# Optimization experiments

Hardware: AMD Instinct MI355X
Metric: run time of the kernel (lower is better)

The kernel has to match this reference:

```python
import jax, jax.numpy as jnp
import numpy as np

B, C, IMG, P = 64, 3, 224, 16
HP = IMG // P                 # 14 patches per side
N = HP * HP                   # 196 patches
R = 196                       # num_superpixels
D, HEADS, DEPTH = 384, 6, 12
HD = D // HEADS
MLP = 4 * D
CLS = 1000
WIN = 4                       # local attention window radius
SEQ = R + 1


def setup_inputs() -> dict:
    key = jax.random.key(0)
    ks = jax.random.split(key, 16)
    nrm = lambda k, s: jax.random.normal(k, s, jnp.float32) * 0.02
    return dict(
        x=jax.random.normal(ks[0], (B, C, IMG, IMG), jnp.float32),
        seg=jax.random.randint(ks[1], (B, IMG, IMG), 0, R, jnp.int32),
        patch_W=nrm(ks[2], (C * P * P, D)), patch_b=jnp.zeros((D,), jnp.float32),
        cls_token=nrm(ks[3], (1, 1, D)),
        pos_W=nrm(ks[4], (2, D)), pos_b=jnp.zeros((D,), jnp.float32),
        cls_pos=nrm(ks[5], (D,)),
        ln1_w=jnp.ones((DEPTH, D), jnp.float32), ln1_b=jnp.zeros((DEPTH, D), jnp.float32),
        qkv_W=nrm(ks[6], (DEPTH, D, 3 * D)), qkv_b=jnp.zeros((DEPTH, 3 * D), jnp.float32),
        proj_W=nrm(ks[7], (DEPTH, D, D)), proj_b=jnp.zeros((DEPTH, D), jnp.float32),
        ln2_w=jnp.ones((DEPTH, D), jnp.float32), ln2_b=jnp.zeros((DEPTH, D), jnp.float32),
        mlp_W1=nrm(ks[8], (DEPTH, D, MLP)), mlp_b1=jnp.zeros((DEPTH, MLP), jnp.float32),
        mlp_W2=nrm(ks[9], (DEPTH, MLP, D)), mlp_b2=jnp.zeros((DEPTH, D), jnp.float32),
        norm_w=jnp.ones((D,), jnp.float32), norm_b=jnp.zeros((D,), jnp.float32),
        head_W=nrm(ks[10], (D, CLS)), head_b=jnp.zeros((CLS,), jnp.float32),
    )


def _ln(x, w, b):
    m = x.mean(-1, keepdims=True)
    v = ((x - m) ** 2).mean(-1, keepdims=True)
    return (x - m) * jax.lax.rsqrt(v + 1e-5) * w + b


def _forward(x, seg, patch_W, patch_b, cls_token, pos_W, pos_b, cls_pos,
             ln1_w, ln1_b, qkv_W, qkv_b, proj_W, proj_b, ln2_w, ln2_b,
             mlp_W1, mlp_b1, mlp_W2, mlp_b2, norm_w, norm_b, head_W, head_b):
    # --- patch embedding (conv stride==kernel == patchify + matmul) -> [B,N,D]
    xp = x.reshape(B, C, HP, P, HP, P).transpose(0, 2, 4, 1, 3, 5).reshape(B, N, C * P * P)
    emb = xp @ patch_W + patch_b
    # --- patch -> superpixel id: segmentation label at patch center pixel
    centers = jnp.arange(HP) * P + P // 2
    patch_seg = seg[:, centers[:, None], centers[None, :]].reshape(B, N)
    # --- mean pooling per superpixel (fused segment reduce over all batches)
    pids = (jnp.arange(B, dtype=patch_seg.dtype)[:, None] * R + patch_seg).reshape(-1)
    sums = jax.ops.segment_sum(emb.reshape(-1, D), pids, num_segments=B * R)
    cnts = jax.ops.segment_sum(jnp.ones((B * N,), emb.dtype), pids, num_segments=B * R)
    pooled = (sums / jnp.maximum(cnts, 1.0)[:, None]).reshape(B, R, D)
    # --- superpixel centroids via pixel-level segment reduce -> [B,R,2] (x,y)
    coords = jnp.arange(IMG, dtype=jnp.float32) / IMG
    yg, xg = jnp.meshgrid(coords, coords, indexing='ij')
    gid = (jnp.arange(B, dtype=seg.dtype)[:, None] * R + seg.reshape(B, -1)).reshape(-1)
    pix = IMG * IMG
    pcnt = jax.ops.segment_sum(jnp.ones((B * pix,), jnp.float32), gid, num_segments=B * R)
    ysum = jax.ops.segment_sum(jnp.broadcast_to(yg.reshape(-1), (B, pix)).reshape(-1), gid, num_segments=B * R)
    xsum = jax.ops.segment_sum(jnp.broadcast_to(xg.reshape(-1), (B, pix)).reshape(-1), gid, num_segments=B * R)
    safe = jnp.maximum(pcnt, 1.0)
    cx = jnp.where(pcnt > 0, xsum / safe, 0.5)
    cy = jnp.where(pcnt > 0, ysum / safe, 0.5)
    centroids = jnp.stack([cx, cy], axis=-1).reshape(B, R, 2)
    # --- prepend cls token, add dynamic (centroid-based) positional encoding
    tok = jnp.concatenate([jnp.broadcast_to(cls_token, (B, 1, D)), pooled], axis=1)
    pos = jnp.concatenate([jnp.broadcast_to(cls_pos[None, None, :], (B, 1, D)),
                           centroids @ pos_W + pos_b], axis=1)
    h = tok + pos
    # --- local (banded) attention mask; cls token attends globally
    idx = jnp.arange(SEQ)
    band = jnp.abs(idx[:, None] - idx[None, :]) <= WIN
    band = band | (idx[:, None] == 0) | (idx[None, :] == 0)
    neg = jnp.float32(-1e9)
    scale = 1.0 / np.sqrt(HD)
    for l in range(DEPTH):
        z = _ln(h, ln1_w[l], ln1_b[l])
        qkv = (z @ qkv_W[l] + qkv_b[l]).reshape(B, SEQ, 3, HEADS, HD)
        q, k, v = qkv[:, :, 0], qkv[:, :, 1], qkv[:, :, 2]
        s = jnp.einsum('bqhd,bkhd->bhqk', q, k) * scale
        s = jnp.where(band[None, None], s, neg)
        a = jax.nn.softmax(s, axis=-1)
        o = jnp.einsum('bhqk,bkhd->bqhd', a, v).reshape(B, SEQ, D)
        h = h + o @ proj_W[l] + proj_b[l]
        z = _ln(h, ln2_w[l], ln2_b[l])
        h = h + jax.nn.gelu(z @ mlp_W1[l] + mlp_b1[l]) @ mlp_W2[l] + mlp_b2[l]
    h = _ln(h, norm_w, norm_b)
    return h[:, 0] @ head_W + head_b


def reference(x, seg, patch_W, patch_b, cls_token, pos_W, pos_b, cls_pos,
              ln1_w, ln1_b, qkv_W, qkv_b, proj_W, proj_b, ln2_w, ln2_b,
              mlp_W1, mlp_b1, mlp_W2, mlp_b2, norm_w, norm_b, head_W, head_b):
    return _forward(x, seg, patch_W, patch_b, cls_token, pos_W, pos_b, cls_pos,
                    ln1_w, ln1_b, qkv_W, qkv_b, proj_W, proj_b, ln2_w, ln2_b,
                    mlp_W1, mlp_b1, mlp_W2, mlp_b2, norm_w, norm_b, head_W, head_b)
```

## Files before the change

kernel.cpp:

```cpp
#include <hip/hip_runtime.h>
#include <hip/hip_bf16.h>
#include <math.h>

typedef unsigned short ushort_t;
typedef unsigned int uint_t;
typedef __attribute__((ext_vector_type(8))) short short8;
typedef __attribute__((ext_vector_type(4))) float f32x4;

#define BATCH 64
#define CHN 3
#define IMG 224
#define PATCH 16
#define HP 14
#define NPATCH 196
#define RSEG 196
#define DMODEL 384
#define HEADS 6
#define HD 64
#define DEPTH 12
#define MLPD 1536
#define CLS 1000
#define WIN 4
#define SEQ 197
#define PIX (IMG*IMG)
#define PATCHK (CHN*PATCH*PATCH)
#define CPARTS 16
#define PPP (PIX / CPARTS)

__device__ __forceinline__ ushort_t f2bf(float f) {
  uint_t u = __float_as_uint(f);
  u += 0x7FFFu + ((u >> 16) & 1u);
  return (ushort_t)(u >> 16);
}
__device__ __forceinline__ float bf2f(ushort_t u) {
  return __uint_as_float((uint_t)u << 16);
}
__device__ __forceinline__ float gelu_tanh(float x) {
  float z = 0.7978845608028654f * (x + 0.044715f * x * x * x);
  z = fminf(fmaxf(z, -15.f), 15.f);
  float t = exp2f(2.8853900817779268f * z);
  return x * t / (t + 1.f);
}
__device__ __forceinline__ int xcd_swizzle(int bid, int nwg) {
  int q = nwg >> 3, r = nwg & 7;
  int xcd = bid & 7, idx = bid >> 3;
  int start = (xcd < r) ? xcd * (q + 1) : r * (q + 1) + (xcd - r) * q;
  return start + idx;
}
__device__ __forceinline__ float dot16bf(const ushort_t* a, const ushort_t* b) {
  const uint_t* a32 = (const uint_t*)a;
  const uint_t* b32 = (const uint_t*)b;
  float acc = 0.f;
#pragma unroll
  for (int w = 0; w < 8; w++) {
    uint_t ka = a32[w], kb = b32[w];
    acc += bf2f((ushort_t)(ka & 0xffff)) * bf2f((ushort_t)(kb & 0xffff));
    acc += bf2f((ushort_t)(ka >> 16)) * bf2f((ushort_t)(kb >> 16));
  }
  return acc;
}

__global__ __launch_bounds__(256) void convtrans_kernel(
    const float* __restrict__ W, ushort_t* __restrict__ Wt, int K, int N) {
  __shared__ float t[32][33];
  int k0 = blockIdx.y * 32, n0 = blockIdx.x * 32;
  const float* Wl = W + (size_t)blockIdx.z * K * N;
  ushort_t* Wtl = Wt + (size_t)blockIdx.z * K * N;
  int tx = threadIdx.x & 31, ty = threadIdx.x >> 5;
#pragma unroll
  for (int i = 0; i < 32; i += 8)
    t[ty + i][tx] = Wl[(size_t)(k0 + ty + i) * N + n0 + tx];
  __syncthreads();
#pragma unroll
  for (int i = 0; i < 32; i += 8)
    Wtl[(size_t)(n0 + ty + i) * K + k0 + tx] = f2bf(t[tx][ty + i]);
}

__global__ __launch_bounds__(256) void patchify_kernel(
    const float* __restrict__ x, ushort_t* __restrict__ xp, int total4) {
  int idx = blockIdx.x * 256 + threadIdx.x;
  if (idx >= total4) return;
  int kq = idx % (PATCHK / 4);
  int m = idx / (PATCHK / 4);
  int n = m % NPATCH;
  int b = m / NPATCH;
  int hi = n / HP, wi = n % HP;
  int k = kq * 4;
  int c = k >> 8;
  int rem = k & 255;
  int pi = rem >> 4, pj = rem & 15;
  int row = hi * PATCH + pi, col = wi * PATCH + pj;
  f32x4 v = *(const f32x4*)&x[(((size_t)b * CHN + c) * IMG + row) * IMG + col];
  uint_t p0 = (uint_t)f2bf(v[0]) | ((uint_t)f2bf(v[1]) << 16);
  uint_t p1 = (uint_t)f2bf(v[2]) | ((uint_t)f2bf(v[3]) << 16);
  uint_t* dst = (uint_t*)(xp + (size_t)idx * 4);
  dst[0] = p0;
  dst[1] = p1;
}

template <int BMT, bool GELU, bool RESID, int OUTMODE>
__global__ __launch_bounds__(256) void gemm_gl(
    const ushort_t* __restrict__ A, const ushort_t* __restrict__ Bt,
    const float* __restrict__ bias, const float* __restrict__ resid,
    void* __restrict__ Cout, int M, int N, int K, int gx) {
  constexpr int AWS = BMT * 2;
  constexpr int AI = AWS / 64;
  constexpr int MF = 4;
  constexpr int NF = (BMT == 128) ? 4 : 2;
  constexpr int BUF_U = (BMT + 128) * 64;
  constexpr int CS_U = BMT * 136;
  constexpr int SMEM_U = (2 * BUF_U > CS_U) ? 2 * BUF_U : CS_U;
  __shared__ __align__(16) ushort_t smem[SMEM_U];
  int tid = threadIdx.x;
  int wave = tid >> 6, lane = tid & 63;
  int flat = xcd_swizzle(blockIdx.x, gridDim.x);
  int bx = flat % gx, by = flat / gx;
  int bm = by * BMT, bn = bx * 128;
  int wr = (BMT == 128) ? (wave >> 1) * 64 : 0;
  int wc = (BMT == 128) ? (wave & 1) * 64 : wave * 32;
  f32x4 acc[MF][NF];
#pragma unroll
  for (int m = 0; m < MF; m++)
#pragma unroll
    for (int n = 0; n < NF; n++)
#pragma unroll
      for (int e = 0; e < 4; e++) acc[m][n][e] = 0.f;

  int r = lane & 15;
  int cfrag = lane >> 4;

  auto STAGE = [&](int buf, int k0) {
    ushort_t* As = smem + buf * BUF_U;
    ushort_t* Bs = As + BMT * 64;
#pragma unroll
    for (int j = 0; j < AI; j++) {
      int s = wave * AWS + j * 64 + lane;
      int row = s >> 3;
      int cp = s & 7;
      int c = cp ^ ((row >> 1) & 7);
      const ushort_t* src = A + (size_t)(bm + row) * K + k0 + c * 8;
      ushort_t* dst = As + (size_t)(wave * AWS + j * 64) * 8;
      __builtin_amdgcn_global_load_lds(
          (const __attribute__((address_space(1))) void*)src,
          (__attribute__((address_space(3))) void*)dst, 16, 0, 0);
    }
#pragma unroll
    for (int j = 0; j < 4; j++) {
      int s = wave * 256 + j * 64 + lane;
      int row = s >> 3;
      int cp = s & 7;
      int c = cp ^ ((row >> 1) & 7);
      const ushort_t* src = Bt + (size_t)(bn + row) * K + k0 + c * 8;
      ushort_t* dst = Bs + (size_t)(wave * 256 + j * 64) * 8;
      __builtin_amdgcn_global_load_lds(
          (const __attribute__((address_space(1))) void*)src,
          (__attribute__((address_space(3))) void*)dst, 16, 0, 0);
    }
  };

  STAGE(0, 0);
  __syncthreads();
  int cur = 0;
  for (int k0 = 0; k0 < K; k0 += 64) {
    if (k0 + 64 < K) STAGE(cur ^ 1, k0 + 64);
    ushort_t* As = smem + cur * BUF_U;
    ushort_t* Bs = As + BMT * 64;
#pragma unroll
    for (int kk = 0; kk < 2; kk++) {
      short8 af[MF], bfr[NF];
#pragma unroll
      for (int m = 0; m < MF; m++) {
        int row = wr + m * 16 + r;
        int sl = (kk * 4 + cfrag) ^ ((row >> 1) & 7);
        af[m] = *(const short8*)(As + row * 64 + sl * 8);
      }
#pragma unroll
      for (int n = 0; n < NF; n++) {
        int row = wc + n * 16 + r;
        int sl = (kk * 4 + cfrag) ^ ((row >> 1) & 7);
        bfr[n] = *(const short8*)(Bs + row * 64 + sl * 8);
      }
      __builtin_amdgcn_s_setprio(1);
#pragma unroll
      for (int m = 0; m < MF; m++)
#pragma unroll
        for (int n = 0; n < NF; n++)
          acc[m][n] = __builtin_amdgcn_mfma_f32_16x16x32_bf16(
              af[m], bfr[n], acc[m][n], 0, 0, 0);
      __builtin_amdgcn_s_setprio(0);
    }
    __syncthreads();
    cur ^= 1;
  }
  int q4 = (lane >> 4) * 4;
  if (OUTMODE == 0) {
#pragma unroll
    for (int n = 0; n < NF; n++) {
      int col = bn + wc + n * 16 + r;
      float bi = bias[col];
#pragma unroll
      for (int m = 0; m < MF; m++) {
#pragma unroll
        for (int e = 0; e < 4; e++) {
          int row = bm + wr + m * 16 + q4 + e;
          if (row < M) {
            float v = acc[m][n][e] + bi;
            if (GELU) v = gelu_tanh(v);
            if (RESID) v += resid[(size_t)row * N + col];
            ((float*)Cout)[(size_t)row * N + col] = v;
          }
        }
      }
    }
  } else {
    ushort_t* Cs = smem;
#pragma unroll
    for (int n = 0; n < NF; n++) {
      int lc = wc + n * 16 + r;
      float bi = bias[bn + lc];
#pragma unroll
      for (int m = 0; m < MF; m++) {
#pragma unroll
        for (int e = 0; e < 4; e++) {
          int lr = wr + m * 16 + q4 + e;
          float v = acc[m][n][e] + bi;
          if (GELU) v = gelu_tanh(v);
          if (RESID) v += resid[(size_t)(bm + lr) * N + bn + lc];
          Cs[lr * 136 + lc] = f2bf(v);
        }
      }
    }
    __syncthreads();
    constexpr int CHUNKS = BMT * 16;
#pragma unroll
    for (int c = 0; c < CHUNKS / 256; c++) {
      int id = c * 256 + tid;
      int row = id >> 4, ch = id & 15;
      int grow = bm + row;
      if (grow < M) {
        short8 val = *(const short8*)(Cs + row * 136 + ch * 8);
        int gcol = bn + ch * 8;
        if (OUTMODE == 1) {
          *(short8*)((ushort_t*)Cout + (size_t)grow * N + gcol) = val;
        } else {
          int b_ = grow / SEQ, t_ = grow - b_ * SEQ;
          int which = gcol / DMODEL;
          int hcol = gcol - which * DMODEL;
          int hh = hcol >> 6, d0 = hcol & 63;
          *(short8*)((ushort_t*)Cout +
                     ((((size_t)b_ * 3 + which) * HEADS + hh) * SEQ + t_) * 64 +
                     d0) = val;
        }
      }
    }
  }
}

__global__ __launch_bounds__(256) void zeroacc_kernel(int* __restrict__ g,
                                                      int n) {
  int i = blockIdx.x * 256 + threadIdx.x;
  if (i < n) g[i] = 0;
}

__global__ __launch_bounds__(256) void centroid_part_kernel(
    const int* __restrict__ seg, int* __restrict__ gacc) {
  __shared__ int cnt[RSEG], si[RSEG], sj[RSEG];
  int b = blockIdx.x, part = blockIdx.y, tid = threadIdx.x;
  for (int r = tid; r < RSEG; r += 256) { cnt[r] = 0; si[r] = 0; sj[r] = 0; }
  __syncthreads();
  const int* s = seg + (size_t)b * PIX;
  int p0 = part * PPP;
  for (int p = p0 + tid; p < p0 + PPP; p += 256) {
    int r = s[p];
    int i = p / IMG, j = p % IMG;
    atomicAdd(&cnt[r], 1);
    atomicAdd(&si[r], i);
    atomicAdd(&sj[r], j);
  }
  __syncthreads();
  for (int r = tid; r < RSEG; r += 256) {
    int c = cnt[r];
    if (c | si[r] | sj[r]) {
      int* g = gacc + ((size_t)b * RSEG + r) * 3;
      atomicAdd(&g[0], c);
      atomicAdd(&g[1], si[r]);
      atomicAdd(&g[2], sj[r]);
    }
  }
}
__global__ __launch_bounds__(256) void centroid_fin_kernel(
    const int* __restrict__ gacc, float* __restrict__ cent) {
  int b = blockIdx.x, tid = threadIdx.x;
  for (int r = tid; r < RSEG; r += 256) {
    const int* g = gacc + ((size_t)b * RSEG + r) * 3;
    int c = g[0];
    float cx = 0.5f, cy = 0.5f;
    if (c > 0) {
      cx = ((float)g[2] / (float)IMG) / (float)c;
      cy = ((float)g[1] / (float)IMG) / (float)c;
    }
    cent[((size_t)b * RSEG + r) * 2 + 0] = cx;
    cent[((size_t)b * RSEG + r) * 2 + 1] = cy;
  }
}

__global__ __launch_bounds__(256) void patchseg_kernel(
    const int* __restrict__ seg, int* __restrict__ pseg) {
  int idx = blockIdx.x * 256 + threadIdx.x;
  if (idx >= BATCH * NPATCH) return;
  int n = idx % NPATCH, b = idx / NPATCH;
  int hi = n / HP, wi = n % HP;
  pseg[idx] = seg[(size_t)b * PIX + (8 + hi * PATCH) * IMG + (8 + wi * PATCH)];
}

__global__ __launch_bounds__(64) void buildlists_kernel(
    const int* __restrict__ pseg, int* __restrict__ starts,
    int* __restrict__ lists) {
  __shared__ int cnt[RSEG];
  int b = blockIdx.x;
  if (threadIdx.x != 0) return;
  const int* ps = pseg + b * NPATCH;
  for (int r = 0; r < RSEG; r++) cnt[r] = 0;
  for (int n = 0; n < NPATCH; n++) cnt[ps[n]]++;
  int run = 0;
  int* st = starts + b * (RSEG + 1);
  for (int r = 0; r < RSEG; r++) {
    st[r] = run;
    int c = cnt[r];
    cnt[r] = run;
    run += c;
  }
  st[RSEG] = run;
  int* li = lists + b * NPATCH;
  for (int n = 0; n < NPATCH; n++) {
    int r = ps[n];
    li[cnt[r]++] = n;
  }
}

__global__ __launch_bounds__(384) void pool_assemble_kernel(
    const float* __restrict__ emb, const float* __restrict__ cent,
    const int* __restrict__ starts, const int* __restrict__ lists,
    const float* __restrict__ cls_token, const float* __restrict__ cls_pos,
    const float* __restrict__ pos_W, const float* __restrict__ pos_b,
    float* __restrict__ h) {
  int t = blockIdx.x;
  int b = t / SEQ, s = t % SEQ;
  int d = threadIdx.x;
  float out;
  if (s == 0) {
    out = cls_token[d] + cls_pos[d];
  } else {
    int r = s - 1;
    int st = starts[b * (RSEG + 1) + r];
    int en = starts[b * (RSEG + 1) + r + 1];
    float acc = 0.f;
    for (int i = st; i < en; i++) {
      int n = lists[b * NPATCH + i];
      acc += emb[((size_t)b * NPATCH + n) * DMODEL + d];
    }
    int cnt = en - st;
    float pooled = acc / (float)(cnt > 0 ? cnt : 1);
    float cx = cent[((size_t)b * RSEG + r) * 2 + 0];
    float cy = cent[((size_t)b * RSEG + r) * 2 + 1];
    out = pooled + cx * pos_W[d] + cy * pos_W[DMODEL + d] + pos_b[d];
  }
  h[(size_t)t * DMODEL + d] = out;
}

template <bool OUTBF16>
__global__ __launch_bounds__(256) void ln_kernel(
    const float* __restrict__ in, void* __restrict__ out,
    const float* __restrict__ w, const float* __restrict__ b, int inStride) {
  int wave = threadIdx.x >> 6, lane = threadIdx.x & 63;
  int row = blockIdx.x * 4 + wave;
  const float* xr = in + (size_t)row * inStride;
  float2 v0 = *(const float2*)(xr + lane * 2);
  float2 v1 = *(const float2*)(xr + 128 + lane * 2);
  float2 v2 = *(const float2*)(xr + 256 + lane * 2);
  float s = v0.x + v0.y + v1.x + v1.y + v2.x + v2.y;
  float s2 = v0.x * v0.x + v0.y * v0.y + v1.x * v1.x + v1.y * v1.y +
             v2.x * v2.x + v2.y * v2.y;
#pragma unroll
  for (int off = 32; off; off >>= 1) {
    s += __shfl_xor(s, off);
    s2 += __shfl_xor(s2, off);
  }
  float m = s / (float)DMODEL;
  float var = s2 / (float)DMODEL - m * m;
  float rs = rsqrtf(var + 1e-5f);
#pragma unroll
  for (int i = 0; i < 3; i++) {
    int d0 = i * 128 + lane * 2;
    float x0 = (i == 0) ? v0.x : (i == 1) ? v1.x : v2.x;
    float x1 = (i == 0) ? v0.y : (i == 1) ? v1.y : v2.y;
    float o0 = (x0 - m) * rs * w[d0] + b[d0];
    float o1 = (x1 - m) * rs * w[d0 + 1] + b[d0 + 1];
    if (OUTBF16) {
      uint_t pack = (uint_t)f2bf(o0) | ((uint_t)f2bf(o1) << 16);
      *(uint_t*)((ushort_t*)out + (size_t)row * DMODEL + d0) = pack;
    } else {
      float2 pk = {o0, o1};
      *(float2*)((float*)out + (size_t)row * DMODEL + d0) = pk;
    }
  }
}

__global__ __launch_bounds__(256) void attn_kernel(
    const ushort_t* __restrict__ qkvp, ushort_t* __restrict__ o) {
  int wave = threadIdx.x >> 6, lane = threadIdx.x & 63;
  int gi = blockIdx.x * 4 + wave;
  int hh = blockIdx.y, b = blockIdx.z;
  const size_t hstride = (size_t)HEADS * SEQ * 64;
  size_t base0 = ((size_t)b * 3 * HEADS + hh) * SEQ * 64;
  const ushort_t* Qh = qkvp + base0;
  const ushort_t* Kh = qkvp + base0 + hstride;
  const ushort_t* Vh = qkvp + base0 + 2 * hstride;
  if (gi < 49) {
    int q0 = 1 + gi * 4;
    int base = q0 - 4;
    if (base < 1) base = 1;
    int row = lane >> 2, dq = lane & 3;
    int key = (row == 0) ? 0 : base + row - 1;
    bool rowvalid = (key <= 196);
    int kaddr = rowvalid ? key : 196;
    const uint_t* kp = (const uint_t*)(Kh + (size_t)kaddr * 64 + dq * 16);
    uint_t kf[8];
#pragma unroll
    for (int w = 0; w < 8; w++) kf[w] = kp[w];
    float v[16];
#pragma unroll
    for (int r = 0; r < 16; r++) {
      int kr = (r == 0) ? 0 : base + r - 1;
      if (kr > 196) kr = 196;
      v[r] = bf2f(Vh[(size_t)kr * 64 + lane]);
    }
#pragma unroll
    for (int i = 0; i < 4; i++) {
      int qi = q0 + i;
      const uint_t* qp = (const uint_t*)(Qh + (size_t)qi * 64 + dq * 16);
      float part = 0.f;
#pragma unroll
      for (int w = 0; w < 8; w++) {
        uint_t ka = kf[w], qa = qp[w];
        part += bf2f((ushort_t)(ka & 0xffff)) * bf2f((ushort_t)(qa & 0xffff));
        part += bf2f((ushort_t)(ka >> 16)) * bf2f((ushort_t)(qa >> 16));
      }
      part += __shfl_xor(part, 1);
      part += __shfl_xor(part, 2);
      int lo = qi - WIN;
      if (lo < 1) lo = 1;
      int hi = qi + WIN;
      if (hi > 196) hi = 196;
      bool valid = rowvalid && ((key == 0) || (key >= lo && key <= hi));
      float s = valid ? part * 0.125f : -1e30f;
      float mx = s;
      mx = fmaxf(mx, __shfl_xor(mx, 4));
      mx = fmaxf(mx, __shfl_xor(mx, 8));
      mx = fmaxf(mx, __shfl_xor(mx, 16));
      mx = fmaxf(mx, __shfl_xor(mx, 32));
      float p = valid ? expf(s - mx) : 0.f;
      float sum = p;
      sum += __shfl_xor(sum, 4);
      sum += __shfl_xor(sum, 8);
      sum += __shfl_xor(sum, 16);
      sum += __shfl_xor(sum, 32);
      float acc = 0.f;
#pragma unroll
      for (int r = 0; r < 16; r++) acc += __shfl(p, r * 4) * v[r];
      o[((size_t)(b * SEQ + qi)) * DMODEL + hh * HD + lane] = f2bf(acc / sum);
    }
  } else if (gi == 49) {
    const ushort_t* qr = Qh;
    float sc0 = -1e30f, sc1 = -1e30f, sc2 = -1e30f, sc3 = -1e30f;
#pragma unroll
    for (int c = 0; c < 4; c++) {
      int key = c * 64 + lane;
      float s = -1e30f;
      if (key < SEQ) {
        const ushort_t* kr = Kh + (size_t)key * 64;
        float acc = dot16bf(kr, qr) + dot16bf(kr + 16, qr + 16) +
                    dot16bf(kr + 32, qr + 32) + dot16bf(kr + 48, qr + 48);
        s = acc * 0.125f;
      }
      if (c == 0) sc0 = s; else if (c == 1) sc1 = s; else if (c == 2) sc2 = s; else sc3 = s;
    }
    float mx = fmaxf(fmaxf(sc0, sc1), fmaxf(sc2, sc3));
#pragma unroll
    for (int off = 32; off; off >>= 1) mx = fmaxf(mx, __shfl_xor(mx, off));
    float p0 = expf(sc0 - mx), p1 = expf(sc1 - mx);
    float p2 = expf(sc2 - mx), p3 = expf(sc3 - mx);
    float sum = p0 + p1 + p2 + p3;
#pragma unroll
    for (int off = 32; off; off >>= 1) sum += __shfl_xor(sum, off);
    float acc = 0.f;
#pragma unroll
    for (int c = 0; c < 4; c++) {
      float pc = (c == 0) ? p0 : (c == 1) ? p1 : (c == 2) ? p2 : p3;
      int jmax = (c < 3) ? 64 : (SEQ - 192);
      for (int jj = 0; jj < jmax; ++jj) {
        float pt = __shfl(pc, jj);
        acc += pt * bf2f(Vh[(size_t)(c * 64 + jj) * 64 + lane]);
      }
    }
    o[((size_t)(b * SEQ)) * DMODEL + hh * HD + lane] = f2bf(acc / sum);
  }
}

__global__ __launch_bounds__(256) void head_kernel(
    const float* __restrict__ hn, const float* __restrict__ W,
    const float* __restrict__ bias, float* __restrict__ out) {
  __shared__ float hs[DMODEL];
  int b = blockIdx.y;
  int c = blockIdx.x * 256 + threadIdx.x;
  for (int d = threadIdx.x; d < DMODEL; d += 256)
    hs[d] = hn[(size_t)b * DMODEL + d];
  __syncthreads();
  if (c >= CLS) return;
  float acc = bias[c];
  for (int d = 0; d < DMODEL; d++) acc += hs[d] * W[(size_t)d * CLS + c];
  out[(size_t)b * CLS + c] = acc;
}

extern "C" void kernel_launch(void* const* d_in, const int* in_sizes, int n_in,
                              void* d_out, int out_size, void* d_ws,
                              size_t ws_size, hipStream_t stream) {
  const float* x = (const float*)d_in[0];
  const int* seg = (const int*)d_in[1];
  const float* patch_W = (const float*)d_in[2];
  const float* patch_b = (const float*)d_in[3];
  const float* cls_token = (const float*)d_in[4];
  const float* pos_W = (const float*)d_in[5];
  const float* pos_b = (const float*)d_in[6];
  const float* cls_pos = (const float*)d_in[7];
  const float* ln1_w = (const float*)d_in[8];
  const float* ln1_b = (const float*)d_in[9];
  const float* qkv_W = (const float*)d_in[10];
  const float* qkv_b = (const float*)d_in[11];
  const float* proj_W = (const float*)d_in[12];
  const float* proj_b = (const float*)d_in[13];
  const float* ln2_w = (const float*)d_in[14];
  const float* ln2_b = (const float*)d_in[15];
  const float* mlp_W1 = (const float*)d_in[16];
  const float* mlp_b1 = (const float*)d_in[17];
  const float* mlp_W2 = (const float*)d_in[18];
  const float* mlp_b2 = (const float*)d_in[19];
  const float* norm_w = (const float*)d_in[20];
  const float* norm_b = (const float*)d_in[21];
  const float* head_W = (const float*)d_in[22];
  const float* head_b = (const float*)d_in[23];
  float* out = (float*)d_out;

  const int M0 = BATCH * NPATCH;
  const int MT = BATCH * SEQ;

  char* ws = (char*)d_ws;
  size_t off = 0;
  auto alloc = [&](size_t bytes) { char* p = ws + off; off += (bytes + 255) & ~(size_t)255; return p; };
  ushort_t* patch_Wt = (ushort_t*)alloc((size_t)PATCHK * DMODEL * 2);
  ushort_t* qkv_Wt   = (ushort_t*)alloc((size_t)DEPTH * DMODEL * 3 * DMODEL * 2);
  ushort_t* proj_Wt  = (ushort_t*)alloc((size_t)DEPTH * DMODEL * DMODEL * 2);
  ushort_t* mlp1_Wt  = (ushort_t*)alloc((size_t)DEPTH * DMODEL * MLPD * 2);
  ushort_t* mlp2_Wt  = (ushort_t*)alloc((size_t)DEPTH * MLPD * DMODEL * 2);
  char* big = alloc((size_t)MT * MLPD * 2);
  ushort_t* xp_bf = (ushort_t*)big;
  ushort_t* mlph_bf = (ushort_t*)big;
  ushort_t* qkvb = (ushort_t*)alloc((size_t)MT * 3 * DMODEL * 2);
  char* eo = alloc((size_t)M0 * DMODEL * 4);
  float* emb = (float*)eo;
  ushort_t* attno = (ushort_t*)eo;
  float* h = (float*)alloc((size_t)MT * DMODEL * 4);
  ushort_t* z_bf = (ushort_t*)alloc((size_t)MT * DMODEL * 2);
  float* cent = (float*)alloc((size_t)BATCH * RSEG * 2 * 4);
  float* hn = (float*)alloc((size_t)BATCH * DMODEL * 4);
  int* pseg = (int*)alloc((size_t)BATCH * NPATCH * 4);
  int* starts = (int*)alloc((size_t)BATCH * (RSEG + 1) * 4);
  int* lists = (int*)alloc((size_t)BATCH * NPATCH * 4);
  int* gacc = (int*)alloc((size_t)BATCH * RSEG * 3 * 4);

  convtrans_kernel<<<dim3(DMODEL / 32, PATCHK / 32, 1), 256, 0, stream>>>(
      patch_W, patch_Wt, PATCHK, DMODEL);
  convtrans_kernel<<<dim3(3 * DMODEL / 32, DMODEL / 32, DEPTH), 256, 0, stream>>>(
      qkv_W, qkv_Wt, DMODEL, 3 * DMODEL);
  convtrans_kernel<<<dim3(DMODEL / 32, DMODEL / 32, DEPTH), 256, 0, stream>>>(
      proj_W, proj_Wt, DMODEL, DMODEL);
  convtrans_kernel<<<dim3(MLPD / 32, DMODEL / 32, DEPTH), 256, 0, stream>>>(
      mlp_W1, mlp1_Wt, DMODEL, MLPD);
  convtrans_kernel<<<dim3(DMODEL / 32, MLPD / 32, DEPTH), 256, 0, stream>>>(
      mlp_W2, mlp2_Wt, MLPD, DMODEL);

  {
    int total4 = M0 * PATCHK / 4;
    patchify_kernel<<<(total4 + 255) / 256, 256, 0, stream>>>(x, xp_bf, total4);
  }
  gemm_gl<64, false, false, 0><<<(DMODEL / 128) * (M0 / 64), 256, 0, stream>>>(
      xp_bf, patch_Wt, patch_b, nullptr, emb, M0, DMODEL, PATCHK, DMODEL / 128);
  {
    int n = BATCH * RSEG * 3;
    zeroacc_kernel<<<(n + 255) / 256, 256, 0, stream>>>(gacc, n);
  }
  centroid_part_kernel<<<dim3(BATCH, CPARTS), 256, 0, stream>>>(seg, gacc);
  centroid_fin_kernel<<<BATCH, 256, 0, stream>>>(gacc, cent);
  patchseg_kernel<<<(M0 + 255) / 256, 256, 0, stream>>>(seg, pseg);
  buildlists_kernel<<<BATCH, 64, 0, stream>>>(pseg, starts, lists);
  pool_assemble_kernel<<<MT, 384, 0, stream>>>(emb, cent, starts, lists,
                                               cls_token, cls_pos, pos_W,
                                               pos_b, h);

  int gy128 = (MT + 127) / 128;
  int gy64 = MT / 64;
  for (int l = 0; l < DEPTH; l++) {
    ln_kernel<true><<<MT / 4, 256, 0, stream>>>(h, z_bf, ln1_w + l * DMODEL,
                                                ln1_b + l * DMODEL, DMODEL);
    gemm_gl<128, false, false, 2><<<(3 * DMODEL / 128) * gy128, 256, 0, stream>>>(
        z_bf, qkv_Wt + (size_t)l * DMODEL * 3 * DMODEL, qkv_b + l * 3 * DMODEL,
        nullptr, qkvb, MT, 3 * DMODEL, DMODEL, 3 * DMODEL / 128);
    attn_kernel<<<dim3(13, HEADS, BATCH), 256, 0, stream>>>(qkvb, attno);
    gemm_gl<64, false, true, 0><<<(DMODEL / 128) * gy64, 256, 0, stream>>>(
        attno, proj_Wt + (size_t)l * DMODEL * DMODEL, proj_b + l * DMODEL, h,
        h, MT, DMODEL, DMODEL, DMODEL / 128);
    ln_kernel<true><<<MT / 4, 256, 0, stream>>>(h, z_bf, ln2_w + l * DMODEL,
                                                ln2_b + l * DMODEL, DMODEL);
    gemm_gl<128, true, false, 1><<<(MLPD / 128) * gy128, 256, 0, stream>>>(
        z_bf, mlp1_Wt + (size_t)l * DMODEL * MLPD, mlp_b1 + l * MLPD, nullptr,
        mlph_bf, MT, MLPD, DMODEL, MLPD / 128);
    gemm_gl<64, false, true, 0><<<(DMODEL / 128) * gy64, 256, 0, stream>>>(
        mlph_bf, mlp2_Wt + (size_t)l * MLPD * DMODEL, mlp_b2 + l * DMODEL, h,
        h, MT, DMODEL, MLPD, DMODEL / 128);
  }
  ln_kernel<false><<<BATCH / 4, 256, 0, stream>>>(h, hn, norm_w, norm_b,
                                                  SEQ * DMODEL);
  head_kernel<<<dim3((CLS + 255) / 256, BATCH), 256, 0, stream>>>(
      hn, head_W, head_b, out);
}
```

Before: 1.926 ms.

## Halve GEMM K-tile to 32 and stage bf16 epilogue in halves to cut LDS

The GEMM K step drops from 64 to 32, which halves each double-buffered A/B stage in shared memory and changes the XOR swizzle to 4 chunks per row. The bf16 epilogue now goes through a 64-row staging buffer one half at a time, so it no longer needs a full BMT-row buffer. Together these cut the kernel's LDS footprint, so more blocks can run per CU. The cost is twice as many K iterations and barriers, fewer MFMAs between syncs, and an extra barrier in the epilogue.

```diff
diff --git a/kernel.cpp b/kernel.cpp
--- a/kernel.cpp
+++ b/kernel.cpp
@@ -103,12 +103,12 @@
     const ushort_t* __restrict__ A, const ushort_t* __restrict__ Bt,
     const float* __restrict__ bias, const float* __restrict__ resid,
     void* __restrict__ Cout, int M, int N, int K, int gx) {
-  constexpr int AWS = BMT * 2;
-  constexpr int AI = AWS / 64;
+  constexpr int AI = BMT / 64;
   constexpr int MF = 4;
   constexpr int NF = (BMT == 128) ? 4 : 2;
-  constexpr int BUF_U = (BMT + 128) * 64;
-  constexpr int CS_U = BMT * 136;
+  constexpr int HALVES = BMT / 64;
+  constexpr int BUF_U = (BMT + 128) * 32;
+  constexpr int CS_U = 64 * 136;
   constexpr int SMEM_U = (2 * BUF_U > CS_U) ? 2 * BUF_U : CS_U;
   __shared__ __align__(16) ushort_t smem[SMEM_U];
   int tid = threadIdx.x;
@@ -131,27 +131,27 @@
 
   auto STAGE = [&](int buf, int k0) {
     ushort_t* As = smem + buf * BUF_U;
-    ushort_t* Bs = As + BMT * 64;
+    ushort_t* Bs = As + BMT * 32;
 #pragma unroll
     for (int j = 0; j < AI; j++) {
-      int s = wave * AWS + j * 64 + lane;
-      int row = s >> 3;
-      int cp = s & 7;
-      int c = cp ^ ((row >> 1) & 7);
+      int s = wave * BMT + j * 64 + lane;
+      int row = s >> 2;
+      int cp = s & 3;
+      int c = cp ^ ((row >> 1) & 3);
       const ushort_t* src = A + (size_t)(bm + row) * K + k0 + c * 8;
-      ushort_t* dst = As + (size_t)(wave * AWS + j * 64) * 8;
+      ushort_t* dst = As + (size_t)(wave * BMT + j * 64) * 8;
       __builtin_amdgcn_global_load_lds(
           (const __attribute__((address_space(1))) void*)src,
           (__attribute__((address_space(3))) void*)dst, 16, 0, 0);
     }
 #pragma unroll
-    for (int j = 0; j < 4; j++) {
-      int s = wave * 256 + j * 64 + lane;
-      int row = s >> 3;
-      int cp = s & 7;
-      int c = cp ^ ((row >> 1) & 7);
+    for (int j = 0; j < 2; j++) {
+      int s = wave * 128 + j * 64 + lane;
+      int row = s >> 2;
+      int cp = s & 3;
+      int c = cp ^ ((row >> 1) & 3);
       const ushort_t* src = Bt + (size_t)(bn + row) * K + k0 + c * 8;
-      ushort_t* dst = Bs + (size_t)(wave * 256 + j * 64) * 8;
+      ushort_t* dst = Bs + (size_t)(wave * 128 + j * 64) * 8;
       __builtin_amdgcn_global_load_lds(
           (const __attribute__((address_space(1))) void*)src,
           (__attribute__((address_space(3))) void*)dst, 16, 0, 0);
@@ -161,34 +161,31 @@
   STAGE(0, 0);
   __syncthreads();
   int cur = 0;
-  for (int k0 = 0; k0 < K; k0 += 64) {
-    if (k0 + 64 < K) STAGE(cur ^ 1, k0 + 64);
+  for (int k0 = 0; k0 < K; k0 += 32) {
+    if (k0 + 32 < K) STAGE(cur ^ 1, k0 + 32);
     ushort_t* As = smem + cur * BUF_U;
-    ushort_t* Bs = As + BMT * 64;
-#pragma unroll
-    for (int kk = 0; kk < 2; kk++) {
-      short8 af[MF], bfr[NF];
-#pragma unroll
-      for (int m = 0; m < MF; m++) {
-        int row = wr + m * 16 + r;
-        int sl = (kk * 4 + cfrag) ^ ((row >> 1) & 7);
-        af[m] = *(const short8*)(As + row * 64 + sl * 8);
-      }
-#pragma unroll
-      for (int n = 0; n < NF; n++) {
-        int row = wc + n * 16 + r;
-        int sl = (kk * 4 + cfrag) ^ ((row >> 1) & 7);
-        bfr[n] = *(const short8*)(Bs + row * 64 + sl * 8);
-      }
-      __builtin_amdgcn_s_setprio(1);
-#pragma unroll
-      for (int m = 0; m < MF; m++)
-#pragma unroll
-        for (int n = 0; n < NF; n++)
-          acc[m][n] = __builtin_amdgcn_mfma_f32_16x16x32_bf16(
-              af[m], bfr[n], acc[m][n], 0, 0, 0);
-      __builtin_amdgcn_s_setprio(0);
-    }
+    ushort_t* Bs = As + BMT * 32;
+    short8 af[MF], bfr[NF];
+#pragma unroll
+    for (int m = 0; m < MF; m++) {
+      int row = wr + m * 16 + r;
+      int sl = cfrag ^ ((row >> 1) & 3);
+      af[m] = *(const short8*)(As + row * 32 + sl * 8);
+    }
+#pragma unroll
+    for (int n = 0; n < NF; n++) {
+      int row = wc + n * 16 + r;
+      int sl = cfrag ^ ((row >> 1) & 3);
+      bfr[n] = *(const short8*)(Bs + row * 32 + sl * 8);
+    }
+    __builtin_amdgcn_s_setprio(1);
+#pragma unroll
+    for (int m = 0; m < MF; m++)
+#pragma unroll
+      for (int n = 0; n < NF; n++)
+        acc[m][n] = __builtin_amdgcn_mfma_f32_16x16x32_bf16(
+            af[m], bfr[n], acc[m][n], 0, 0, 0);
+    __builtin_amdgcn_s_setprio(0);
     __syncthreads();
     cur ^= 1;
   }
@@ -215,43 +212,50 @@
   } else {
     ushort_t* Cs = smem;
 #pragma unroll
-    for (int n = 0; n < NF; n++) {
-      int lc = wc + n * 16 + r;
-      float bi = bias[bn + lc];
-#pragma unroll
-      for (int m = 0; m < MF; m++) {
-#pragma unroll
-        for (int e = 0; e < 4; e++) {
-          int lr = wr + m * 16 + q4 + e;
-          float v = acc[m][n][e] + bi;
-          if (GELU) v = gelu_tanh(v);
-          if (RESID) v += resid[(size_t)(bm + lr) * N + bn + lc];
-          Cs[lr * 136 + lc] = f2bf(v);
+    for (int p = 0; p < HALVES; p++) {
+      if (wr == p * 64) {
+#pragma unroll
+        for (int n = 0; n < NF; n++) {
+          int lc = wc + n * 16 + r;
+          float bi = bias[bn + lc];
+#pragma unroll
+          for (int m = 0; m < MF; m++) {
+#pragma unroll
+            for (int e = 0; e < 4; e++) {
+              int lr = m * 16 + q4 + e;
+              float v = acc[m][n][e] + bi;
+              if (GELU) v = gelu_tanh(v);
+              if (RESID)
+                v += resid[(size_t)(bm + p * 64 + lr) * N + bn + lc];
+              Cs[lr * 136 + lc] = f2bf(v);
+            }
+          }
         }
       }
-    }
-    __syncthreads();
-    constexpr int CHUNKS = BMT * 16;
-#pragma unroll
-    for (int c = 0; c < CHUNKS / 256; c++) {
-      int id = c * 256 + tid;
-      int row = id >> 4, ch = id & 15;
-      int grow = bm + row;
-      if (grow < M) {
-        short8 val = *(const short8*)(Cs + row * 136 + ch * 8);
-        int gcol = bn + ch * 8;
-        if (OUTMODE == 1) {
-          *(short8*)((ushort_t*)Cout + (size_t)grow * N + gcol) = val;
-        } else {
-          int b_ = grow / SEQ, t_ = grow - b_ * SEQ;
-          int which = gcol / DMODEL;
-          int hcol = gcol - which * DMODEL;
-          int hh = hcol >> 6, d0 = hcol & 63;
-          *(short8*)((ushort_t*)Cout +
-                     ((((size_t)b_ * 3 + which) * HEADS + hh) * SEQ + t_) * 64 +
-                     d0) = val;
+      __syncthreads();
+#pragma unroll
+      for (int c = 0; c < 4; c++) {
+        int id = c * 256 + tid;
+        int row = id >> 4, ch = id & 15;
+        int grow = bm + p * 64 + row;
+        if (grow < M) {
+          short8 val = *(const short8*)(Cs + row * 136 + ch * 8);
+          int gcol = bn + ch * 8;
+          if (OUTMODE == 1) {
+            *(short8*)((ushort_t*)Cout + (size_t)grow * N + gcol) = val;
+          } else {
+            int b_ = grow / SEQ, t_ = grow - b_ * SEQ;
+            int which = gcol / DMODEL;
+            int hcol = gcol - which * DMODEL;
+            int hh = hcol >> 6, d0 = hcol & 63;
+            *(short8*)((ushort_t*)Cout +
+                       ((((size_t)b_ * 3 + which) * HEADS + hh) * SEQ + t_) *
+                           64 +
+                       d0) = val;
+          }
         }
       }
+      if (p + 1 < HALVES) __syncthreads();
     }
   }
 }
```

After: 2.206 ms. +14.5%, slower.
